# Kernel optimization log

Measured on AMD Instinct MI355X. Metric: run time of the kernel, lower is better.

The kernel has to match this reference:

```python
import jax, jax.numpy as jnp
import numpy as np

N = 100000      # nodes
E = 1600000     # edges (before self-loops)
IN = 128        # in_channels
HID = 64        # hidden_channels (= out_channels)
HEADS = 8
CH = HID // HEADS  # per-head channels in GAT (concat=True)


def setup_inputs() -> dict:
    key = jax.random.key(0)
    ks = jax.random.split(key, 12)
    s = 0.1  # param init scale
    return {
        "x": jax.random.normal(ks[0], (N, IN), jnp.float32),
        "edge_index": jax.random.randint(ks[1], (2, E), 0, N, dtype=jnp.int32),
        # GCNConv 0: in -> hid
        "W0": s * jax.random.normal(ks[2], (IN, HID), jnp.float32),
        "b0": jnp.zeros((HID,), jnp.float32),
        # GATConv: hid -> heads x ch (concat)
        "Wg": s * jax.random.normal(ks[3], (HID, HEADS * CH), jnp.float32),
        "att_src": s * jax.random.normal(ks[4], (HEADS, CH), jnp.float32),
        "att_dst": s * jax.random.normal(ks[5], (HEADS, CH), jnp.float32),
        "bg": jnp.zeros((HEADS * CH,), jnp.float32),
        # GCNConv 2: hid -> hid
        "W2": s * jax.random.normal(ks[6], (HID, HID), jnp.float32),
        "b2": jnp.zeros((HID,), jnp.float32),
        # GCNConv 3 (final): hid -> out
        "W3": s * jax.random.normal(ks[7], (HID, HID), jnp.float32),
        "b3": jnp.zeros((HID,), jnp.float32),
    }


def _gcn_conv(x, src, dst, W, b, n):
    deg = jax.ops.segment_sum(jnp.ones(src.shape[0], x.dtype), dst, num_segments=n)
    dinv = jnp.where(deg > 0, jax.lax.rsqrt(deg), 0.0)
    h = x @ W                                  # [n, out]
    norm = dinv[src] * dinv[dst]               # [e]
    msg = h[src] * norm[:, None]               # gather + scale
    return jax.ops.segment_sum(msg, dst, num_segments=n) + b


def _gat_conv(x, src, dst, W, a_src, a_dst, b, n):
    # PyG GATConv (v1), concat=True, negative_slope=0.2, self-loops in src/dst
    h = (x @ W).reshape(n, HEADS, CH)          # [n, H, C]
    alpha_src = jnp.sum(h * a_src, axis=-1)    # [n, H]
    alpha_dst = jnp.sum(h * a_dst, axis=-1)    # [n, H]
    e = jax.nn.leaky_relu(alpha_src[src] + alpha_dst[dst], 0.2)  # [E, H]
    # softmax over incoming edges of each destination node
    m = jax.ops.segment_max(e, dst, num_segments=n)              # [n, H]
    p = jnp.exp(e - m[dst])
    z = jax.ops.segment_sum(p, dst, num_segments=n)              # [n, H]
    alpha = p / z[dst]                                           # [E, H]
    out = jax.ops.segment_sum(alpha[:, :, None] * h[src], dst, num_segments=n)  # [n, H, C]
    return out.reshape(n, HEADS * CH) + b


def reference(x, edge_index, W0, b0, Wg, att_src, att_dst, bg, W2, b2, W3, b3):
    n = x.shape[0]
    loops = jnp.arange(n, dtype=edge_index.dtype)
    src = jnp.concatenate([edge_index[0], loops])
    dst = jnp.concatenate([edge_index[1], loops])
    # GCN -> relu -> GAT -> relu -> GCN -> relu -> GCN  (dropout p=0.0 is identity)
    h = jax.nn.relu(_gcn_conv(x, src, dst, W0, b0, n))
    h = jax.nn.relu(_gat_conv(h, src, dst, Wg, att_src, att_dst, bg, n))
    h = jax.nn.relu(_gcn_conv(h, src, dst, W2, b2, n))
    h = _gcn_conv(h, src, dst, W3, b3, n)
    return h
```

## Files before the change

kernel.cpp:

```cpp
#include <hip/hip_runtime.h>
#include <hip/hip_bf16.h>


__device__ __forceinline__ float leaky02(float x) { return x > 0.0f ? x : 0.2f * x; }
__device__ __forceinline__ unsigned short f2bf(float f) {
  unsigned u = __float_as_uint(f);
  u += 0x7FFFu + ((u >> 16) & 1u);
  return (unsigned short)(u >> 16);
}
__device__ __forceinline__ float bflo(unsigned d) { return __uint_as_float(d << 16); }
__device__ __forceinline__ float bfhi(unsigned d) { return __uint_as_float(d & 0xFFFF0000u); }

#define NB_PART 64

__global__ __launch_bounds__(1024) void hist_kernel(
    const int* __restrict__ dst, int* __restrict__ hist, int ne, int nbkt) {
  __shared__ int h[512];
  const int tid = threadIdx.x;
  for (int i = tid; i < 512; i += 1024) h[i] = 0;
  __syncthreads();
  const int chunk = (ne + NB_PART - 1) / NB_PART;
  const int beg = blockIdx.x * chunk;
  const int end = min(beg + chunk, ne);
  for (int e = beg + tid; e < end; e += 1024) atomicAdd(&h[dst[e] >> 8], 1);
  __syncthreads();
  for (int i = tid; i < nbkt; i += 1024) hist[blockIdx.x * nbkt + i] = h[i];
}

__global__ __launch_bounds__(512) void pscan_kernel(
    int* __restrict__ hist, int* __restrict__ bktBase, int nbkt, int ne) {
  __shared__ int tot[512];
  const int t = threadIdx.x;
  int run = 0;
  if (t < nbkt) {
    for (int b = 0; b < NB_PART; ++b) {
      int v = hist[b * nbkt + t];
      hist[b * nbkt + t] = run;
      run += v;
    }
  }
  tot[t] = (t < nbkt) ? run : 0;
  __syncthreads();
  for (int off = 1; off < 512; off <<= 1) {
    int u = (t >= off) ? tot[t - off] : 0;
    __syncthreads();
    tot[t] += u;
    __syncthreads();
  }
  if (t < nbkt) bktBase[t] = tot[t] - run;
  if (t == 0) bktBase[nbkt] = ne;
}

__global__ __launch_bounds__(1024) void part_kernel(
    const int* __restrict__ src, const int* __restrict__ dst,
    const int* __restrict__ hist, const int* __restrict__ bktBase,
    int2* __restrict__ part, int ne, int nbkt) {
  __shared__ int cur[512];
  const int tid = threadIdx.x;
  for (int i = tid; i < nbkt; i += 1024)
    cur[i] = bktBase[i] + hist[blockIdx.x * nbkt + i];
  __syncthreads();
  const int chunk = (ne + NB_PART - 1) / NB_PART;
  const int beg = blockIdx.x * chunk;
  const int end = min(beg + chunk, ne);
  for (int e = beg + tid; e < end; e += 1024) {
    int d = dst[e];
    int s = src[e];
    int pos = atomicAdd(&cur[d >> 8], 1);
    part[pos] = make_int2(s, d);
  }
}

__global__ __launch_bounds__(256) void build_kernel(
    const int2* __restrict__ part, const int* __restrict__ bktBase,
    int* __restrict__ rowptr, int* __restrict__ csr, float* __restrict__ dinv,
    int n, int ne) {
  __shared__ int cnt[256], sc[256], cur[256];
  const int b = blockIdx.x, tid = threadIdx.x;
  const int lo = b << 8;
  const int ebeg = bktBase[b], eend = bktBase[b + 1];
  cnt[tid] = 0;
  __syncthreads();
  for (int e = ebeg + tid; e < eend; e += 256) atomicAdd(&cnt[part[e].y - lo], 1);
  __syncthreads();
  sc[tid] = cnt[tid];
  __syncthreads();
  for (int off = 1; off < 256; off <<= 1) {
    int u = (tid >= off) ? sc[tid - off] : 0;
    __syncthreads();
    sc[tid] += u;
    __syncthreads();
  }
  const int excl = sc[tid] - cnt[tid];
  const int node = lo + tid;
  if (node < n) {
    rowptr[node] = ebeg + excl;
    dinv[node] = rsqrtf((float)(cnt[tid] + 1));
  }
  cur[tid] = ebeg + excl;
  __syncthreads();
  for (int e = ebeg + tid; e < eend; e += 256) {
    int2 p = part[e];
    int pos = atomicAdd(&cur[p.y - lo], 1);
    csr[pos] = p.x;
  }
  if (b == 0 && tid == 0) rowptr[n] = ne;
}

template<int K, bool SCALE>
__global__ __launch_bounds__(256) void matmul_kernel(
    const float* __restrict__ A, const float* __restrict__ W,
    const float* __restrict__ dinv, unsigned short* __restrict__ C, int n) {
  __shared__ float sW[K * 64];
  __shared__ float sA[64 * (K + 1)];
  const int tid = threadIdx.x;
  const int row0 = blockIdx.x * 64;
  for (int i = tid; i < K * 16; i += 256)
    reinterpret_cast<float4*>(sW)[i] = reinterpret_cast<const float4*>(W)[i];
  const int f4r = K / 4;
  for (int i = tid; i < 64 * f4r; i += 256) {
    int r = i / f4r, f = i - r * f4r;
    int row = row0 + r;
    float4 v = (row < n)
        ? reinterpret_cast<const float4*>(&A[(long)row * K])[f]
        : make_float4(0.f, 0.f, 0.f, 0.f);
    float* p = &sA[r * (K + 1) + f * 4];
    p[0] = v.x; p[1] = v.y; p[2] = v.z; p[3] = v.w;
  }
  __syncthreads();
  const int tc = tid & 15, tr = tid >> 4;
  const int c0 = tc * 4, r0 = tr * 4;
  float4 acc0 = {0,0,0,0}, acc1 = {0,0,0,0}, acc2 = {0,0,0,0}, acc3 = {0,0,0,0};
  const float* a0 = &sA[(r0 + 0) * (K + 1)];
  const float* a1 = &sA[(r0 + 1) * (K + 1)];
  const float* a2 = &sA[(r0 + 2) * (K + 1)];
  const float* a3 = &sA[(r0 + 3) * (K + 1)];
#pragma unroll 8
  for (int k = 0; k < K; ++k) {
    float4 w = *reinterpret_cast<const float4*>(&sW[k * 64 + c0]);
    float x0 = a0[k], x1 = a1[k], x2 = a2[k], x3 = a3[k];
    acc0.x = fmaf(x0, w.x, acc0.x); acc0.y = fmaf(x0, w.y, acc0.y);
    acc0.z = fmaf(x0, w.z, acc0.z); acc0.w = fmaf(x0, w.w, acc0.w);
    acc1.x = fmaf(x1, w.x, acc1.x); acc1.y = fmaf(x1, w.y, acc1.y);
    acc1.z = fmaf(x1, w.z, acc1.z); acc1.w = fmaf(x1, w.w, acc1.w);
    acc2.x = fmaf(x2, w.x, acc2.x); acc2.y = fmaf(x2, w.y, acc2.y);
    acc2.z = fmaf(x2, w.z, acc2.z); acc2.w = fmaf(x2, w.w, acc2.w);
    acc3.x = fmaf(x3, w.x, acc3.x); acc3.y = fmaf(x3, w.y, acc3.y);
    acc3.z = fmaf(x3, w.z, acc3.z); acc3.w = fmaf(x3, w.w, acc3.w);
  }
  float4 accs[4] = {acc0, acc1, acc2, acc3};
#pragma unroll
  for (int i = 0; i < 4; ++i) {
    int row = row0 + r0 + i;
    if (row < n) {
      float s = SCALE ? dinv[row] : 1.0f;
      unsigned short q0 = f2bf(accs[i].x * s), q1 = f2bf(accs[i].y * s);
      unsigned short q2 = f2bf(accs[i].z * s), q3 = f2bf(accs[i].w * s);
      uint2 o;
      o.x = (unsigned)q0 | ((unsigned)q1 << 16);
      o.y = (unsigned)q2 | ((unsigned)q3 << 16);
      *reinterpret_cast<uint2*>(&C[(long)row * 64 + c0]) = o;
    }
  }
}

template<bool RELU>
__global__ __launch_bounds__(256) void gcn_layer_kernel(
    const int* __restrict__ rowptr, const int* __restrict__ csr,
    const unsigned short* __restrict__ hs, const float* __restrict__ dinv,
    const float* __restrict__ bias, float* __restrict__ out, int n) {
  int node = blockIdx.x * 4 + (threadIdx.x >> 6);
  if (node >= n) return;
  int lane = threadIdx.x & 63;
  int slot = lane >> 3;
  int li = lane & 7;
  int c0 = li * 8;
  int beg = rowptr[node], end = rowptr[node + 1];
  float4 accA = {0,0,0,0}, accB = {0,0,0,0};
  int j = beg;
  int idx = (j + li < end) ? csr[j + li] : 0;
  while (j < end) {
    int s = __shfl(idx, slot);
    bool valid = (j + slot) < end;
    int jn = j + 8;
    if (jn < end) idx = (jn + li < end) ? csr[jn + li] : 0;
    if (valid) {
      uint4 v = *reinterpret_cast<const uint4*>(&hs[(long)s * 64 + c0]);
      accA.x += bflo(v.x); accA.y += bfhi(v.x);
      accA.z += bflo(v.y); accA.w += bfhi(v.y);
      accB.x += bflo(v.z); accB.y += bfhi(v.z);
      accB.z += bflo(v.w); accB.w += bfhi(v.w);
    }
    j = jn;
  }
  if (slot == 0) {
    uint4 v = *reinterpret_cast<const uint4*>(&hs[(long)node * 64 + c0]);
    accA.x += bflo(v.x); accA.y += bfhi(v.x);
    accA.z += bflo(v.y); accA.w += bfhi(v.y);
    accB.x += bflo(v.z); accB.y += bfhi(v.z);
    accB.z += bflo(v.w); accB.w += bfhi(v.w);
  }
#pragma unroll
  for (int m = 8; m <= 32; m <<= 1) {
    accA.x += __shfl_xor(accA.x, m); accA.y += __shfl_xor(accA.y, m);
    accA.z += __shfl_xor(accA.z, m); accA.w += __shfl_xor(accA.w, m);
    accB.x += __shfl_xor(accB.x, m); accB.y += __shfl_xor(accB.y, m);
    accB.z += __shfl_xor(accB.z, m); accB.w += __shfl_xor(accB.w, m);
  }
  if (slot == 0) {
    float sdv = dinv[node];
    float4 bbA = *reinterpret_cast<const float4*>(&bias[c0]);
    float4 bbB = *reinterpret_cast<const float4*>(&bias[c0 + 4]);
    float4 oA = make_float4(fmaf(sdv, accA.x, bbA.x), fmaf(sdv, accA.y, bbA.y),
                            fmaf(sdv, accA.z, bbA.z), fmaf(sdv, accA.w, bbA.w));
    float4 oB = make_float4(fmaf(sdv, accB.x, bbB.x), fmaf(sdv, accB.y, bbB.y),
                            fmaf(sdv, accB.z, bbB.z), fmaf(sdv, accB.w, bbB.w));
    if (RELU) {
      oA.x = fmaxf(oA.x, 0.f); oA.y = fmaxf(oA.y, 0.f);
      oA.z = fmaxf(oA.z, 0.f); oA.w = fmaxf(oA.w, 0.f);
      oB.x = fmaxf(oB.x, 0.f); oB.y = fmaxf(oB.y, 0.f);
      oB.z = fmaxf(oB.z, 0.f); oB.w = fmaxf(oB.w, 0.f);
    }
    *reinterpret_cast<float4*>(&out[(long)node * 64 + c0]) = oA;
    *reinterpret_cast<float4*>(&out[(long)node * 64 + c0 + 4]) = oB;
  }
}

__global__ void gat_alpha_kernel(
    const unsigned short* __restrict__ hg, const float* __restrict__ att_src,
    const float* __restrict__ att_dst,
    float* __restrict__ asrc, float* __restrict__ adst, int total) {
  int i = blockIdx.x * 256 + threadIdx.x;
  if (i >= total) return;
  int nrow = i >> 3, h = i & 7;
  uint4 v = *reinterpret_cast<const uint4*>(&hg[(long)nrow * 64 + h * 8]);
  float f[8] = {bflo(v.x), bfhi(v.x), bflo(v.y), bfhi(v.y),
                bflo(v.z), bfhi(v.z), bflo(v.w), bfhi(v.w)};
  float ss = 0.f, dd = 0.f;
#pragma unroll
  for (int c = 0; c < 8; ++c) {
    ss = fmaf(f[c], att_src[h * 8 + c], ss);
    dd = fmaf(f[c], att_dst[h * 8 + c], dd);
  }
  asrc[i] = ss;
  adst[i] = dd;
}

__global__ __launch_bounds__(256) void gat_layer_kernel(
    const int* __restrict__ rowptr, const int* __restrict__ csr,
    const unsigned short* __restrict__ hg, const float* __restrict__ asrc,
    const float* __restrict__ adst, const float* __restrict__ bg,
    float* __restrict__ out, int n) {
  int node = blockIdx.x * 4 + (threadIdx.x >> 6);
  if (node >= n) return;
  int lane = threadIdx.x & 63;
  int slot = lane >> 3;
  int li = lane & 7;
  int c0 = li * 8;
  int h = li;
  int beg = rowptr[node], end = rowptr[node + 1];
  float adn = adst[node * 8 + h];
  float4 accA = {0,0,0,0}, accB = {0,0,0,0};
  float z = 0.f;
  int j = beg;
  int idx = (j + li < end) ? csr[j + li] : 0;
  while (j < end) {
    int s = __shfl(idx, slot);
    bool valid = (j + slot) < end;
    int jn = j + 8;
    if (jn < end) idx = (jn + li < end) ? csr[jn + li] : 0;
    if (valid) {
      float p = __expf(leaky02(asrc[s * 8 + h] + adn));
      uint4 v = *reinterpret_cast<const uint4*>(&hg[(long)s * 64 + c0]);
      z += p;
      accA.x = fmaf(p, bflo(v.x), accA.x); accA.y = fmaf(p, bfhi(v.x), accA.y);
      accA.z = fmaf(p, bflo(v.y), accA.z); accA.w = fmaf(p, bfhi(v.y), accA.w);
      accB.x = fmaf(p, bflo(v.z), accB.x); accB.y = fmaf(p, bfhi(v.z), accB.y);
      accB.z = fmaf(p, bflo(v.w), accB.z); accB.w = fmaf(p, bfhi(v.w), accB.w);
    }
    j = jn;
  }
  if (slot == 0) {
    float p = __expf(leaky02(asrc[node * 8 + h] + adn));
    uint4 v = *reinterpret_cast<const uint4*>(&hg[(long)node * 64 + c0]);
    z += p;
    accA.x = fmaf(p, bflo(v.x), accA.x); accA.y = fmaf(p, bfhi(v.x), accA.y);
    accA.z = fmaf(p, bflo(v.y), accA.z); accA.w = fmaf(p, bfhi(v.y), accA.w);
    accB.x = fmaf(p, bflo(v.z), accB.x); accB.y = fmaf(p, bfhi(v.z), accB.y);
    accB.z = fmaf(p, bflo(v.w), accB.z); accB.w = fmaf(p, bfhi(v.w), accB.w);
  }
#pragma unroll
  for (int m = 8; m <= 32; m <<= 1) {
    accA.x += __shfl_xor(accA.x, m); accA.y += __shfl_xor(accA.y, m);
    accA.z += __shfl_xor(accA.z, m); accA.w += __shfl_xor(accA.w, m);
    accB.x += __shfl_xor(accB.x, m); accB.y += __shfl_xor(accB.y, m);
    accB.z += __shfl_xor(accB.z, m); accB.w += __shfl_xor(accB.w, m);
    z += __shfl_xor(z, m);
  }
  if (slot == 0) {
    float rz = 1.0f / z;
    float4 bbA = *reinterpret_cast<const float4*>(&bg[c0]);
    float4 bbB = *reinterpret_cast<const float4*>(&bg[c0 + 4]);
    float4 oA = make_float4(fmaxf(fmaf(accA.x, rz, bbA.x), 0.f),
                            fmaxf(fmaf(accA.y, rz, bbA.y), 0.f),
                            fmaxf(fmaf(accA.z, rz, bbA.z), 0.f),
                            fmaxf(fmaf(accA.w, rz, bbA.w), 0.f));
    float4 oB = make_float4(fmaxf(fmaf(accB.x, rz, bbB.x), 0.f),
                            fmaxf(fmaf(accB.y, rz, bbB.y), 0.f),
                            fmaxf(fmaf(accB.z, rz, bbB.z), 0.f),
                            fmaxf(fmaf(accB.w, rz, bbB.w), 0.f));
    *reinterpret_cast<float4*>(&out[(long)node * 64 + c0]) = oA;
    *reinterpret_cast<float4*>(&out[(long)node * 64 + c0 + 4]) = oB;
  }
}

extern "C" void kernel_launch(void* const* d_in, const int* in_sizes, int n_in,
                              void* d_out, int out_size, void* d_ws, size_t ws_size,
                              hipStream_t stream) {
  const float* x  = (const float*)d_in[0];
  const int* ei   = (const int*)d_in[1];
  const float* W0 = (const float*)d_in[2];
  const float* b0 = (const float*)d_in[3];
  const float* Wg = (const float*)d_in[4];
  const float* av = (const float*)d_in[5];
  const float* aw = (const float*)d_in[6];
  const float* bg = (const float*)d_in[7];
  const float* W2 = (const float*)d_in[8];
  const float* b2 = (const float*)d_in[9];
  const float* W3 = (const float*)d_in[10];
  const float* b3 = (const float*)d_in[11];

  const int N = in_sizes[0] / 128;
  const int E = in_sizes[1] / 2;
  const int* src = ei;
  const int* dst = ei + E;
  const int nbkt = (N + 255) >> 8;

  char* base = (char*)d_ws;
  size_t off = 0;
  auto alloc = [&](size_t bytes) {
    void* p = base + off;
    off = (off + bytes + 255) & ~(size_t)255;
    return p;
  };
  int*   hist    = (int*)alloc((size_t)NB_PART * nbkt * 4);
  int*   bktBase = (int*)alloc((size_t)(nbkt + 1) * 4);
  int*   rowptr  = (int*)alloc((size_t)(N + 1) * 4);
  int*   csr     = (int*)alloc((size_t)E * 4);
  float* dinv    = (float*)alloc((size_t)N * 4);
  float* as_     = (float*)alloc((size_t)N * 8 * 4);
  float* ad_     = (float*)alloc((size_t)N * 8 * 4);
  unsigned short* fA = (unsigned short*)alloc((size_t)N * 64 * 4);
  float* bufB    = (float*)alloc((size_t)N * 64 * 4);
  int2*  part    = (int2*)fA;
  (void)ws_size; (void)n_in; (void)out_size;

  const int gN8   = (N * 8 + 255) / 256;
  const int gMM   = (N + 63) / 64;
  const int gNode = (N + 3) / 4;

  hist_kernel<<<NB_PART, 1024, 0, stream>>>(dst, hist, E, nbkt);
  pscan_kernel<<<1, 512, 0, stream>>>(hist, bktBase, nbkt, E);
  part_kernel<<<NB_PART, 1024, 0, stream>>>(src, dst, hist, bktBase, part, E, nbkt);
  build_kernel<<<nbkt, 256, 0, stream>>>(part, bktBase, rowptr, csr, dinv, N, E);

  matmul_kernel<128, true><<<gMM, 256, 0, stream>>>(x, W0, dinv, fA, N);
  gcn_layer_kernel<true><<<gNode, 256, 0, stream>>>(rowptr, csr, fA, dinv, b0, bufB, N);

  matmul_kernel<64, false><<<gMM, 256, 0, stream>>>(bufB, Wg, nullptr, fA, N);
  gat_alpha_kernel<<<gN8, 256, 0, stream>>>(fA, av, aw, as_, ad_, N * 8);
  gat_layer_kernel<<<gNode, 256, 0, stream>>>(rowptr, csr, fA, as_, ad_, bg, bufB, N);

  matmul_kernel<64, true><<<gMM, 256, 0, stream>>>(bufB, W2, dinv, fA, N);
  gcn_layer_kernel<true><<<gNode, 256, 0, stream>>>(rowptr, csr, fA, dinv, b2, bufB, N);

  matmul_kernel<64, true><<<gMM, 256, 0, stream>>>(bufB, W3, dinv, fA, N);
  gcn_layer_kernel<false><<<gNode, 256, 0, stream>>>(rowptr, csr, fA, dinv, b3,
                                                     (float*)d_out, N);
}
```

Measured before the change: 467.3 us.

## Pack CSR partition, store intermediates in bf16, fuse GAT alpha, slice GAT features

The partition entries are packed into 32 bits (24-bit source plus the 8-bit local dst), halving partition traffic. Intermediate activations between layers are stored as bf16 instead of fp32, and the matmul reads bf16 inputs. The GAT attention logits are computed in the matmul epilogue, which removes gat_alpha_kernel. GAT features are stored in head-pair slices with a transposed alpha layout, and the GAT kernel walks 32 edges per wave per slice to improve gather locality. Nontemporal loads are added for the edge streams. The cost is extra bf16 rounding of intermediates and 24-bit source indices, which limits N to about 16M nodes.

Measured after the change: 621.1 us. 32.9% more time.

```diff
diff --git a/kernel.cpp b/kernel.cpp
--- a/kernel.cpp
+++ b/kernel.cpp
@@ -8,6 +8,9 @@
   u += 0x7FFFu + ((u >> 16) & 1u);
   return (unsigned short)(u >> 16);
 }
+__device__ __forceinline__ unsigned pkbf(float a, float b) {
+  return (unsigned)f2bf(a) | ((unsigned)f2bf(b) << 16);
+}
 __device__ __forceinline__ float bflo(unsigned d) { return __uint_as_float(d << 16); }
 __device__ __forceinline__ float bfhi(unsigned d) { return __uint_as_float(d & 0xFFFF0000u); }
 
@@ -22,7 +25,8 @@
   const int chunk = (ne + NB_PART - 1) / NB_PART;
   const int beg = blockIdx.x * chunk;
   const int end = min(beg + chunk, ne);
-  for (int e = beg + tid; e < end; e += 1024) atomicAdd(&h[dst[e] >> 8], 1);
+  for (int e = beg + tid; e < end; e += 1024)
+    atomicAdd(&h[__builtin_nontemporal_load(&dst[e]) >> 8], 1);
   __syncthreads();
   for (int i = tid; i < nbkt; i += 1024) hist[blockIdx.x * nbkt + i] = h[i];
 }
@@ -54,7 +58,7 @@
 __global__ __launch_bounds__(1024) void part_kernel(
     const int* __restrict__ src, const int* __restrict__ dst,
     const int* __restrict__ hist, const int* __restrict__ bktBase,
-    int2* __restrict__ part, int ne, int nbkt) {
+    unsigned* __restrict__ part, int ne, int nbkt) {
   __shared__ int cur[512];
   const int tid = threadIdx.x;
   for (int i = tid; i < nbkt; i += 1024)
@@ -64,15 +68,15 @@
   const int beg = blockIdx.x * chunk;
   const int end = min(beg + chunk, ne);
   for (int e = beg + tid; e < end; e += 1024) {
-    int d = dst[e];
-    int s = src[e];
+    int d = __builtin_nontemporal_load(&dst[e]);
+    int s = __builtin_nontemporal_load(&src[e]);
     int pos = atomicAdd(&cur[d >> 8], 1);
-    part[pos] = make_int2(s, d);
+    part[pos] = (unsigned)s | ((unsigned)(d & 255) << 24);
   }
 }
 
 __global__ __launch_bounds__(256) void build_kernel(
-    const int2* __restrict__ part, const int* __restrict__ bktBase,
+    const unsigned* __restrict__ part, const int* __restrict__ bktBase,
     int* __restrict__ rowptr, int* __restrict__ csr, float* __restrict__ dinv,
     int n, int ne) {
   __shared__ int cnt[256], sc[256], cur[256];
@@ -81,7 +85,7 @@
   const int ebeg = bktBase[b], eend = bktBase[b + 1];
   cnt[tid] = 0;
   __syncthreads();
-  for (int e = ebeg + tid; e < eend; e += 256) atomicAdd(&cnt[part[e].y - lo], 1);
+  for (int e = ebeg + tid; e < eend; e += 256) atomicAdd(&cnt[part[e] >> 24], 1);
   __syncthreads();
   sc[tid] = cnt[tid];
   __syncthreads();
@@ -100,32 +104,50 @@
   cur[tid] = ebeg + excl;
   __syncthreads();
   for (int e = ebeg + tid; e < eend; e += 256) {
-    int2 p = part[e];
-    int pos = atomicAdd(&cur[p.y - lo], 1);
-    csr[pos] = p.x;
+    unsigned p = part[e];
+    int pos = atomicAdd(&cur[p >> 24], 1);
+    csr[pos] = (int)(p & 0x00FFFFFFu);
   }
   if (b == 0 && tid == 0) rowptr[n] = ne;
 }
 
-template<int K, bool SCALE>
+template<int K, bool SCALE, bool ABF16, int OMODE>
 __global__ __launch_bounds__(256) void matmul_kernel(
-    const float* __restrict__ A, const float* __restrict__ W,
-    const float* __restrict__ dinv, unsigned short* __restrict__ C, int n) {
+    const void* __restrict__ Ain, const float* __restrict__ W,
+    const float* __restrict__ dinv, unsigned short* __restrict__ C,
+    const float* __restrict__ attS, const float* __restrict__ attD,
+    float* __restrict__ asT, float* __restrict__ adT, int n) {
   __shared__ float sW[K * 64];
   __shared__ float sA[64 * (K + 1)];
   const int tid = threadIdx.x;
   const int row0 = blockIdx.x * 64;
   for (int i = tid; i < K * 16; i += 256)
     reinterpret_cast<float4*>(sW)[i] = reinterpret_cast<const float4*>(W)[i];
-  const int f4r = K / 4;
-  for (int i = tid; i < 64 * f4r; i += 256) {
-    int r = i / f4r, f = i - r * f4r;
-    int row = row0 + r;
-    float4 v = (row < n)
-        ? reinterpret_cast<const float4*>(&A[(long)row * K])[f]
-        : make_float4(0.f, 0.f, 0.f, 0.f);
-    float* p = &sA[r * (K + 1) + f * 4];
-    p[0] = v.x; p[1] = v.y; p[2] = v.z; p[3] = v.w;
+  if constexpr (!ABF16) {
+    const float* A = (const float*)Ain;
+    const int f4r = K / 4;
+    for (int i = tid; i < 64 * f4r; i += 256) {
+      int r = i / f4r, f = i - r * f4r;
+      int row = row0 + r;
+      float4 v = (row < n)
+          ? reinterpret_cast<const float4*>(&A[(long)row * K])[f]
+          : make_float4(0.f, 0.f, 0.f, 0.f);
+      float* p = &sA[r * (K + 1) + f * 4];
+      p[0] = v.x; p[1] = v.y; p[2] = v.z; p[3] = v.w;
+    }
+  } else {
+    const unsigned short* A = (const unsigned short*)Ain;
+    const int f8r = K / 8;
+    for (int i = tid; i < 64 * f8r; i += 256) {
+      int r = i / f8r, f = i - r * f8r;
+      int row = row0 + r;
+      uint4 v = (row < n)
+          ? *reinterpret_cast<const uint4*>(&A[(long)row * K + f * 8])
+          : make_uint4(0, 0, 0, 0);
+      float* p = &sA[r * (K + 1) + f * 8];
+      p[0] = bflo(v.x); p[1] = bfhi(v.x); p[2] = bflo(v.y); p[3] = bfhi(v.y);
+      p[4] = bflo(v.z); p[5] = bfhi(v.z); p[6] = bflo(v.w); p[7] = bfhi(v.w);
+    }
   }
   __syncthreads();
   const int tc = tid & 15, tr = tid >> 4;
@@ -152,23 +174,44 @@
 #pragma unroll
   for (int i = 0; i < 4; ++i) {
     int row = row0 + r0 + i;
-    if (row < n) {
-      float s = SCALE ? dinv[row] : 1.0f;
-      unsigned short q0 = f2bf(accs[i].x * s), q1 = f2bf(accs[i].y * s);
-      unsigned short q2 = f2bf(accs[i].z * s), q3 = f2bf(accs[i].w * s);
-      uint2 o;
-      o.x = (unsigned)q0 | ((unsigned)q1 << 16);
-      o.y = (unsigned)q2 | ((unsigned)q3 << 16);
-      *reinterpret_cast<uint2*>(&C[(long)row * 64 + c0]) = o;
-    }
-  }
-}
-
-template<bool RELU>
+    float s = SCALE ? ((row < n) ? dinv[row] : 1.0f) : 1.0f;
+    float v0 = accs[i].x * s, v1 = accs[i].y * s;
+    float v2 = accs[i].z * s, v3 = accs[i].w * s;
+    if constexpr (OMODE == 1) {
+      float ps = fmaf(v0, attS[c0], fmaf(v1, attS[c0 + 1],
+                 fmaf(v2, attS[c0 + 2], v3 * attS[c0 + 3])));
+      float pd = fmaf(v0, attD[c0], fmaf(v1, attD[c0 + 1],
+                 fmaf(v2, attD[c0 + 2], v3 * attD[c0 + 3])));
+      ps += __shfl_xor(ps, 1);
+      pd += __shfl_xor(pd, 1);
+      if (row < n) {
+        if ((tc & 1) == 0) {
+          int h = c0 >> 3;
+          asT[(long)h * n + row] = ps;
+          adT[(long)h * n + row] = pd;
+        }
+        int sl = c0 >> 4, cc = c0 & 15;
+        uint2 o;
+        o.x = pkbf(v0, v1);
+        o.y = pkbf(v2, v3);
+        *reinterpret_cast<uint2*>(&C[((long)sl * n + row) * 16 + cc]) = o;
+      }
+    } else {
+      if (row < n) {
+        uint2 o;
+        o.x = pkbf(v0, v1);
+        o.y = pkbf(v2, v3);
+        *reinterpret_cast<uint2*>(&C[(long)row * 64 + c0]) = o;
+      }
+    }
+  }
+}
+
+template<bool RELU, bool OBF16>
 __global__ __launch_bounds__(256) void gcn_layer_kernel(
     const int* __restrict__ rowptr, const int* __restrict__ csr,
     const unsigned short* __restrict__ hs, const float* __restrict__ dinv,
-    const float* __restrict__ bias, float* __restrict__ out, int n) {
+    const float* __restrict__ bias, void* __restrict__ out, int n) {
   int node = blockIdx.x * 4 + (threadIdx.x >> 6);
   if (node >= n) return;
   int lane = threadIdx.x & 63;
@@ -211,86 +254,74 @@
     float sdv = dinv[node];
     float4 bbA = *reinterpret_cast<const float4*>(&bias[c0]);
     float4 bbB = *reinterpret_cast<const float4*>(&bias[c0 + 4]);
-    float4 oA = make_float4(fmaf(sdv, accA.x, bbA.x), fmaf(sdv, accA.y, bbA.y),
-                            fmaf(sdv, accA.z, bbA.z), fmaf(sdv, accA.w, bbA.w));
-    float4 oB = make_float4(fmaf(sdv, accB.x, bbB.x), fmaf(sdv, accB.y, bbB.y),
-                            fmaf(sdv, accB.z, bbB.z), fmaf(sdv, accB.w, bbB.w));
+    float o0 = fmaf(sdv, accA.x, bbA.x), o1 = fmaf(sdv, accA.y, bbA.y);
+    float o2 = fmaf(sdv, accA.z, bbA.z), o3 = fmaf(sdv, accA.w, bbA.w);
+    float o4 = fmaf(sdv, accB.x, bbB.x), o5 = fmaf(sdv, accB.y, bbB.y);
+    float o6 = fmaf(sdv, accB.z, bbB.z), o7 = fmaf(sdv, accB.w, bbB.w);
     if (RELU) {
-      oA.x = fmaxf(oA.x, 0.f); oA.y = fmaxf(oA.y, 0.f);
-      oA.z = fmaxf(oA.z, 0.f); oA.w = fmaxf(oA.w, 0.f);
-      oB.x = fmaxf(oB.x, 0.f); oB.y = fmaxf(oB.y, 0.f);
-      oB.z = fmaxf(oB.z, 0.f); oB.w = fmaxf(oB.w, 0.f);
-    }
-    *reinterpret_cast<float4*>(&out[(long)node * 64 + c0]) = oA;
-    *reinterpret_cast<float4*>(&out[(long)node * 64 + c0 + 4]) = oB;
-  }
-}
-
-__global__ void gat_alpha_kernel(
-    const unsigned short* __restrict__ hg, const float* __restrict__ att_src,
-    const float* __restrict__ att_dst,
-    float* __restrict__ asrc, float* __restrict__ adst, int total) {
-  int i = blockIdx.x * 256 + threadIdx.x;
-  if (i >= total) return;
-  int nrow = i >> 3, h = i & 7;
-  uint4 v = *reinterpret_cast<const uint4*>(&hg[(long)nrow * 64 + h * 8]);
-  float f[8] = {bflo(v.x), bfhi(v.x), bflo(v.y), bfhi(v.y),
-                bflo(v.z), bfhi(v.z), bflo(v.w), bfhi(v.w)};
-  float ss = 0.f, dd = 0.f;
-#pragma unroll
-  for (int c = 0; c < 8; ++c) {
-    ss = fmaf(f[c], att_src[h * 8 + c], ss);
-    dd = fmaf(f[c], att_dst[h * 8 + c], dd);
-  }
-  asrc[i] = ss;
-  adst[i] = dd;
+      o0 = fmaxf(o0, 0.f); o1 = fmaxf(o1, 0.f); o2 = fmaxf(o2, 0.f);
+      o3 = fmaxf(o3, 0.f); o4 = fmaxf(o4, 0.f); o5 = fmaxf(o5, 0.f);
+      o6 = fmaxf(o6, 0.f); o7 = fmaxf(o7, 0.f);
+    }
+    if constexpr (OBF16) {
+      unsigned short* op = (unsigned short*)out;
+      uint4 q;
+      q.x = pkbf(o0, o1); q.y = pkbf(o2, o3);
+      q.z = pkbf(o4, o5); q.w = pkbf(o6, o7);
+      *reinterpret_cast<uint4*>(&op[(long)node * 64 + c0]) = q;
+    } else {
+      float* op = (float*)out;
+      *reinterpret_cast<float4*>(&op[(long)node * 64 + c0]) =
+          make_float4(o0, o1, o2, o3);
+      *reinterpret_cast<float4*>(&op[(long)node * 64 + c0 + 4]) =
+          make_float4(o4, o5, o6, o7);
+    }
+  }
 }
 
 __global__ __launch_bounds__(256) void gat_layer_kernel(
     const int* __restrict__ rowptr, const int* __restrict__ csr,
-    const unsigned short* __restrict__ hg, const float* __restrict__ asrc,
-    const float* __restrict__ adst, const float* __restrict__ bg,
-    float* __restrict__ out, int n) {
-  int node = blockIdx.x * 4 + (threadIdx.x >> 6);
-  if (node >= n) return;
-  int lane = threadIdx.x & 63;
-  int slot = lane >> 3;
-  int li = lane & 7;
-  int c0 = li * 8;
-  int h = li;
-  int beg = rowptr[node], end = rowptr[node + 1];
-  float adn = adst[node * 8 + h];
+    const unsigned short* __restrict__ hg,
+    const float* __restrict__ asT, const float* __restrict__ adT,
+    const float* __restrict__ bg, unsigned short* __restrict__ out,
+    int n, int halfN) {
+  const int g = blockIdx.x & 7;
+  const int slice = g >> 1, sub = g & 1;
+  const int node = sub * halfN + (blockIdx.x >> 3) * 4 + (threadIdx.x >> 6);
+  const int lim = sub ? n : halfN;
+  if (node >= lim) return;
+  const int lane = threadIdx.x & 63;
+  const int slot = lane >> 1;
+  const int ci = lane & 1;
+  const int h = slice * 2 + ci;
+  const unsigned short* __restrict__ hgs = hg + (long)slice * n * 16;
+  const float* __restrict__ ash = asT + (long)h * n;
+  const float adn = adT[(long)h * n + node];
+  const int beg = rowptr[node], end = rowptr[node + 1];
   float4 accA = {0,0,0,0}, accB = {0,0,0,0};
   float z = 0.f;
   int j = beg;
-  int idx = (j + li < end) ? csr[j + li] : 0;
+  int idx = (lane < 32 && j + lane < end)
+      ? __builtin_nontemporal_load(&csr[j + lane]) : 0;
   while (j < end) {
+    int jn = j + 32;
+    int idxn = (lane < 32 && jn + lane < end)
+        ? __builtin_nontemporal_load(&csr[jn + lane]) : 0;
     int s = __shfl(idx, slot);
-    bool valid = (j + slot) < end;
-    int jn = j + 8;
-    if (jn < end) idx = (jn + li < end) ? csr[jn + li] : 0;
-    if (valid) {
-      float p = __expf(leaky02(asrc[s * 8 + h] + adn));
-      uint4 v = *reinterpret_cast<const uint4*>(&hg[(long)s * 64 + c0]);
+    if (j + slot < end) {
+      float p = __expf(leaky02(ash[s] + adn));
+      uint4 v = *reinterpret_cast<const uint4*>(&hgs[(long)s * 16 + ci * 8]);
       z += p;
       accA.x = fmaf(p, bflo(v.x), accA.x); accA.y = fmaf(p, bfhi(v.x), accA.y);
       accA.z = fmaf(p, bflo(v.y), accA.z); accA.w = fmaf(p, bfhi(v.y), accA.w);
       accB.x = fmaf(p, bflo(v.z), accB.x); accB.y = fmaf(p, bfhi(v.z), accB.y);
       accB.z = fmaf(p, bflo(v.w), accB.z); accB.w = fmaf(p, bfhi(v.w), accB.w);
     }
+    idx = idxn;
     j = jn;
   }
-  if (slot == 0) {
-    float p = __expf(leaky02(asrc[node * 8 + h] + adn));
-    uint4 v = *reinterpret_cast<const uint4*>(&hg[(long)node * 64 + c0]);
-    z += p;
-    accA.x = fmaf(p, bflo(v.x), accA.x); accA.y = fmaf(p, bfhi(v.x), accA.y);
-    accA.z = fmaf(p, bflo(v.y), accA.z); accA.w = fmaf(p, bfhi(v.y), accA.w);
-    accB.x = fmaf(p, bflo(v.z), accB.x); accB.y = fmaf(p, bfhi(v.z), accB.y);
-    accB.z = fmaf(p, bflo(v.w), accB.z); accB.w = fmaf(p, bfhi(v.w), accB.w);
-  }
 #pragma unroll
-  for (int m = 8; m <= 32; m <<= 1) {
+  for (int m = 2; m <= 32; m <<= 1) {
     accA.x += __shfl_xor(accA.x, m); accA.y += __shfl_xor(accA.y, m);
     accA.z += __shfl_xor(accA.z, m); accA.w += __shfl_xor(accA.w, m);
     accB.x += __shfl_xor(accB.x, m); accB.y += __shfl_xor(accB.y, m);
@@ -298,19 +329,29 @@
     z += __shfl_xor(z, m);
   }
   if (slot == 0) {
+    float pS = __expf(leaky02(ash[node] + adn));
+    uint4 v = *reinterpret_cast<const uint4*>(&hgs[(long)node * 16 + ci * 8]);
+    z += pS;
+    accA.x = fmaf(pS, bflo(v.x), accA.x); accA.y = fmaf(pS, bfhi(v.x), accA.y);
+    accA.z = fmaf(pS, bflo(v.y), accA.z); accA.w = fmaf(pS, bfhi(v.y), accA.w);
+    accB.x = fmaf(pS, bflo(v.z), accB.x); accB.y = fmaf(pS, bfhi(v.z), accB.y);
+    accB.z = fmaf(pS, bflo(v.w), accB.z); accB.w = fmaf(pS, bfhi(v.w), accB.w);
     float rz = 1.0f / z;
-    float4 bbA = *reinterpret_cast<const float4*>(&bg[c0]);
-    float4 bbB = *reinterpret_cast<const float4*>(&bg[c0 + 4]);
-    float4 oA = make_float4(fmaxf(fmaf(accA.x, rz, bbA.x), 0.f),
-                            fmaxf(fmaf(accA.y, rz, bbA.y), 0.f),
-                            fmaxf(fmaf(accA.z, rz, bbA.z), 0.f),
-                            fmaxf(fmaf(accA.w, rz, bbA.w), 0.f));
-    float4 oB = make_float4(fmaxf(fmaf(accB.x, rz, bbB.x), 0.f),
-                            fmaxf(fmaf(accB.y, rz, bbB.y), 0.f),
-                            fmaxf(fmaf(accB.z, rz, bbB.z), 0.f),
-                            fmaxf(fmaf(accB.w, rz, bbB.w), 0.f));
-    *reinterpret_cast<float4*>(&out[(long)node * 64 + c0]) = oA;
-    *reinterpret_cast<float4*>(&out[(long)node * 64 + c0 + 4]) = oB;
+    const int c = slice * 16 + ci * 8;
+    float4 bbA = *reinterpret_cast<const float4*>(&bg[c]);
+    float4 bbB = *reinterpret_cast<const float4*>(&bg[c + 4]);
+    float o0 = fmaxf(fmaf(accA.x, rz, bbA.x), 0.f);
+    float o1 = fmaxf(fmaf(accA.y, rz, bbA.y), 0.f);
+    float o2 = fmaxf(fmaf(accA.z, rz, bbA.z), 0.f);
+    float o3 = fmaxf(fmaf(accA.w, rz, bbA.w), 0.f);
+    float o4 = fmaxf(fmaf(accB.x, rz, bbB.x), 0.f);
+    float o5 = fmaxf(fmaf(accB.y, rz, bbB.y), 0.f);
+    float o6 = fmaxf(fmaf(accB.z, rz, bbB.z), 0.f);
+    float o7 = fmaxf(fmaf(accB.w, rz, bbB.w), 0.f);
+    uint4 q;
+    q.x = pkbf(o0, o1); q.y = pkbf(o2, o3);
+    q.z = pkbf(o4, o5); q.w = pkbf(o6, o7);
+    *reinterpret_cast<uint4*>(&out[(long)node * 64 + c]) = q;
   }
 }
 
@@ -335,6 +376,7 @@
   const int* src = ei;
   const int* dst = ei + E;
   const int nbkt = (N + 255) >> 8;
+  const int halfN = (N + 1) >> 1;
 
   char* base = (char*)d_ws;
   size_t off = 0;
@@ -348,33 +390,40 @@
   int*   rowptr  = (int*)alloc((size_t)(N + 1) * 4);
   int*   csr     = (int*)alloc((size_t)E * 4);
   float* dinv    = (float*)alloc((size_t)N * 4);
-  float* as_     = (float*)alloc((size_t)N * 8 * 4);
-  float* ad_     = (float*)alloc((size_t)N * 8 * 4);
-  unsigned short* fA = (unsigned short*)alloc((size_t)N * 64 * 4);
-  float* bufB    = (float*)alloc((size_t)N * 64 * 4);
-  int2*  part    = (int2*)fA;
+  float* asT     = (float*)alloc((size_t)N * 8 * 4);
+  float* adT     = (float*)alloc((size_t)N * 8 * 4);
+  unsigned short* fStd = (unsigned short*)alloc((size_t)N * 64 * 2);
+  unsigned short* fSl  = (unsigned short*)alloc((size_t)N * 64 * 2);
+  unsigned short* aggB = (unsigned short*)alloc((size_t)N * 64 * 2);
+  unsigned* part = (unsigned*)fSl;
   (void)ws_size; (void)n_in; (void)out_size;
 
-  const int gN8   = (N * 8 + 255) / 256;
   const int gMM   = (N + 63) / 64;
   const int gNode = (N + 3) / 4;
+  const int gGat  = 8 * ((halfN + 3) / 4);
 
   hist_kernel<<<NB_PART, 1024, 0, stream>>>(dst, hist, E, nbkt);
   pscan_kernel<<<1, 512, 0, stream>>>(hist, bktBase, nbkt, E);
   part_kernel<<<NB_PART, 1024, 0, stream>>>(src, dst, hist, bktBase, part, E, nbkt);
   build_kernel<<<nbkt, 256, 0, stream>>>(part, bktBase, rowptr, csr, dinv, N, E);
 
-  matmul_kernel<128, true><<<gMM, 256, 0, stream>>>(x, W0, dinv, fA, N);
-  gcn_layer_kernel<true><<<gNode, 256, 0, stream>>>(rowptr, csr, fA, dinv, b0, bufB, N);
-
-  matmul_kernel<64, false><<<gMM, 256, 0, stream>>>(bufB, Wg, nullptr, fA, N);
-  gat_alpha_kernel<<<gN8, 256, 0, stream>>>(fA, av, aw, as_, ad_, N * 8);
-  gat_layer_kernel<<<gNode, 256, 0, stream>>>(rowptr, csr, fA, as_, ad_, bg, bufB, N);
-
-  matmul_kernel<64, true><<<gMM, 256, 0, stream>>>(bufB, W2, dinv, fA, N);
-  gcn_layer_kernel<true><<<gNode, 256, 0, stream>>>(rowptr, csr, fA, dinv, b2, bufB, N);
-
-  matmul_kernel<64, true><<<gMM, 256, 0, stream>>>(bufB, W3, dinv, fA, N);
-  gcn_layer_kernel<false><<<gNode, 256, 0, stream>>>(rowptr, csr, fA, dinv, b3,
-                                                     (float*)d_out, N);
-}
+  matmul_kernel<128, true, false, 0><<<gMM, 256, 0, stream>>>(
+      x, W0, dinv, fStd, nullptr, nullptr, nullptr, nullptr, N);
+  gcn_layer_kernel<true, true><<<gNode, 256, 0, stream>>>(
+      rowptr, csr, fStd, dinv, b0, aggB, N);
+
+  matmul_kernel<64, false, true, 1><<<gMM, 256, 0, stream>>>(
+      aggB, Wg, nullptr, fSl, av, aw, asT, adT, N);
+  gat_layer_kernel<<<gGat, 256, 0, stream>>>(
+      rowptr, csr, fSl, asT, adT, bg, aggB, N, halfN);
+
+  matmul_kernel<64, true, true, 0><<<gMM, 256, 0, stream>>>(
+      aggB, W2, dinv, fStd, nullptr, nullptr, nullptr, nullptr, N);
+  gcn_layer_kernel<true, true><<<gNode, 256, 0, stream>>>(
+      rowptr, csr, fStd, dinv, b2, aggB, N);
+
+  matmul_kernel<64, true, true, 0><<<gMM, 256, 0, stream>>>(
+      aggB, W3, dinv, fStd, nullptr, nullptr, nullptr, nullptr, N);
+  gcn_layer_kernel<false, false><<<gNode, 256, 0, stream>>>(
+      rowptr, csr, fStd, dinv, b3, d_out, N);
+}
```
